# Optimization experiments

Measured on AMD Instinct MI355X. Metric: run time of the kernel, lower is better.

Reference implementation:

```python
import jax, jax.numpy as jnp
import numpy as np

N, E, DIN, ED, H, C = 50000, 800000, 128, 16, 4, 128
HC = H * C
SLOPE = 0.2


def gat_conv(x, ei_src, ei_dst, ea, W, a_src, a_dst, We, a_e, b):
    # x: [N, din]; ea: [E, ed] (self-loops already appended by caller)
    n = x.shape[0]
    h = (x @ W).reshape(n, H, C)                       # [N,H,C]
    al_src = (h * a_src).sum(-1)                       # [N,H]
    al_dst = (h * a_dst).sum(-1)                       # [N,H]
    e = (ea @ We).reshape(-1, H, C)                    # [E,H,C]
    al_e = (e * a_e).sum(-1)                           # [E,H]
    alpha = al_src[ei_src] + al_dst[ei_dst] + al_e     # [E,H]
    alpha = jnp.where(alpha > 0, alpha, SLOPE * alpha)  # LeakyReLU(0.2)
    # per-destination-node segment softmax (stable)
    amax = jax.ops.segment_max(alpha, ei_dst, num_segments=n)
    amax = jnp.where(jnp.isfinite(amax), amax, 0.0)
    ex = jnp.exp(alpha - amax[ei_dst])
    den = jax.ops.segment_sum(ex, ei_dst, num_segments=n)
    alpha = ex / (den[ei_dst] + 1e-16)                 # [E,H]
    msg = h[ei_src] * alpha[:, :, None]                # [E,H,C]
    out = jax.ops.segment_sum(msg, ei_dst, num_segments=n)  # [N,H,C]
    return out.reshape(n, HC) + b


def setup_inputs() -> dict:
    key = jax.random.key(0)
    ks = jax.random.split(key, 16)
    s = 0.05
    inp = {
        "x": jax.random.normal(ks[0], (N, DIN), jnp.float32),
        "edge_index": jax.random.randint(ks[1], (2, E), 0, N, jnp.int64),
        "edge_features": jax.random.normal(ks[2], (E, ED), jnp.float32),
        # layer 1 params
        "W1": jax.random.normal(ks[3], (DIN, HC), jnp.float32) * s,
        "att_src1": jax.random.normal(ks[4], (H, C), jnp.float32) * s,
        "att_dst1": jax.random.normal(ks[5], (H, C), jnp.float32) * s,
        "lin_e1": jax.random.normal(ks[6], (ED, HC), jnp.float32) * s,
        "att_e1": jax.random.normal(ks[7], (H, C), jnp.float32) * s,
        "b1": jnp.zeros((HC,), jnp.float32),
        # layer 2 params
        "W2": jax.random.normal(ks[8], (HC, HC), jnp.float32) * s,
        "att_src2": jax.random.normal(ks[9], (H, C), jnp.float32) * s,
        "att_dst2": jax.random.normal(ks[10], (H, C), jnp.float32) * s,
        "lin_e2": jax.random.normal(ks[11], (ED, HC), jnp.float32) * s,
        "att_e2": jax.random.normal(ks[12], (H, C), jnp.float32) * s,
        "b2": jnp.zeros((HC,), jnp.float32),
    }
    return inp


def reference(x, edge_index, edge_features,
              W1, att_src1, att_dst1, lin_e1, att_e1, b1,
              W2, att_src2, att_dst2, lin_e2, att_e2, b2):
    # add self-loops once (PyG default: add_self_loops=True, edge_attr fill='mean')
    loop = jnp.arange(N, dtype=edge_index.dtype)
    ei_src = jnp.concatenate([edge_index[0], loop])
    ei_dst = jnp.concatenate([edge_index[1], loop])
    mean_ea = edge_features.mean(0)
    ea = jnp.concatenate([edge_features, jnp.broadcast_to(mean_ea, (N, ED))], axis=0)

    h = gat_conv(x, ei_src, ei_dst, ea, W1, att_src1, att_dst1, lin_e1, att_e1, b1)
    h = jax.nn.elu(h)
    h = gat_conv(h, ei_src, ei_dst, ea, W2, att_src2, att_dst2, lin_e2, att_e2, b2)
    return jax.nn.elu(h)
```

## Files before the change

kernel.cpp:

```cpp
#include <hip/hip_runtime.h>
#include <math.h>

#define NNODE 50000
#define NEDGE 800000
#define DINv  128
#define EDv   16
#define NHv   4
#define CHv   128
#define HCv   512
#define SLOPEv 0.2f
#define MEANBLK 512
#define CONVN (NNODE * DINv / 4)

typedef __attribute__((ext_vector_type(8))) short bf16x8;
typedef __attribute__((ext_vector_type(4))) float f32x4;
typedef __attribute__((address_space(3))) unsigned lds_u32;
typedef const __attribute__((address_space(1))) unsigned glb_u32;

__device__ __forceinline__ ushort f2b(float f) {
  unsigned u = __float_as_uint(f);
  u += 0x7FFF + ((u >> 16) & 1);
  return (ushort)(u >> 16);
}
__device__ __forceinline__ float blo(unsigned u) { return __uint_as_float(u << 16); }
__device__ __forceinline__ float bhi(unsigned u) { return __uint_as_float(u & 0xffff0000u); }

__global__ void detect_kernel(const int* __restrict__ ei, int* __restrict__ flag) {
  __shared__ int bad;
  if (threadIdx.x == 0) bad = 0;
  __syncthreads();
  for (int i = threadIdx.x; i < 2048; i += 256)
    if (ei[2 * i + 1] != 0) bad = 1;
  __syncthreads();
  if (threadIdx.x == 0) flag[0] = bad ? 0 : 1;
}

__device__ __forceinline__ int load_idx(const int* __restrict__ ei, int e, int row, int wide) {
  if (wide) return ei[2 * ((size_t)row * NEDGE + e)];
  return ei[(size_t)row * NEDGE + e];
}

__global__ void count_kernel(const int* __restrict__ ei, const int* __restrict__ flag,
                             int* __restrict__ deg) {
  int e = blockIdx.x * blockDim.x + threadIdx.x;
  if (e < NEDGE) {
    int w = flag[0];
    atomicAdd(&deg[load_idx(ei, e, 1, w)], 1);
  }
}

__global__ __launch_bounds__(1024) void scan_kernel(const int* __restrict__ deg,
                                                    int* __restrict__ row_ptr) {
  __shared__ int wsum[16];
  int tid = threadIdx.x;
  int wid = tid >> 6, lane = tid & 63;
  int carry = 0;
  for (int base = 0; base < NNODE; base += 4096) {
    int idx = base + tid * 4;
    int4 x = make_int4(0, 0, 0, 0);
    if (idx < NNODE) x = *(const int4*)(deg + idx);
    int t0 = x.x, t1 = t0 + x.y, t2 = t1 + x.z, t3 = t2 + x.w;
    int v = t3;
#pragma unroll
    for (int off = 1; off < 64; off <<= 1) {
      int t = __shfl_up(v, off, 64);
      if (lane >= off) v += t;
    }
    if (lane == 63) wsum[wid] = v;
    __syncthreads();
    if (wid == 0) {
      int s = (lane < 16) ? wsum[lane] : 0;
#pragma unroll
      for (int off = 1; off < 16; off <<= 1) {
        int t = __shfl_up(s, off, 64);
        if (lane >= off) s += t;
      }
      if (lane < 16) wsum[lane] = s;
    }
    __syncthreads();
    int woff = wid ? wsum[wid - 1] : 0;
    int excl = carry + woff + v - t3;
    if (idx < NNODE) {
      int4 o = make_int4(excl, excl + t0, excl + t1, excl + t2);
      *(int4*)(row_ptr + idx) = o;
    }
    carry += wsum[15];
    __syncthreads();
  }
  if (tid == 0) row_ptr[NNODE] = carry;
}

__global__ void scatter_kernel(const int* __restrict__ ei, const int* __restrict__ flag,
                               const int* __restrict__ row_ptr, int* __restrict__ cursor,
                               int* __restrict__ src_sorted, int* __restrict__ eid_sorted) {
  int e = blockIdx.x * blockDim.x + threadIdx.x;
  if (e < NEDGE) {
    int w = flag[0];
    int d = load_idx(ei, e, 1, w);
    int s = load_idx(ei, e, 0, w);
    int p = row_ptr[d] + atomicAdd(&cursor[d], 1);
    src_sorted[p] = s;
    eid_sorted[p] = e;
  }
}

__global__ void prep_kernel(const float* __restrict__ We1, const float* __restrict__ ae1,
                            const float* __restrict__ We2, const float* __restrict__ ae2,
                            float* __restrict__ v1, float* __restrict__ v2) {
  int t = threadIdx.x;
  int layer = t >> 6, u = t & 63;
  int d = u >> 2, h = u & 3;
  const float* We = layer ? We2 : We1;
  const float* ae = layer ? ae2 : ae1;
  float s = 0.f;
  for (int c = 0; c < CHv; c++) s += We[(size_t)d * HCv + h * CHv + c] * ae[h * CHv + c];
  (layer ? v2 : v1)[d * 4 + h] = s;
}

__global__ void mean_part_kernel(const float* __restrict__ ea, float* __restrict__ partials) {
  float acc[EDv];
#pragma unroll
  for (int d = 0; d < EDv; d++) acc[d] = 0.f;
  int stride = gridDim.x * blockDim.x;
  for (int r = blockIdx.x * blockDim.x + threadIdx.x; r < NEDGE; r += stride) {
    const float4* p = (const float4*)(ea + (size_t)r * EDv);
#pragma unroll
    for (int q = 0; q < 4; q++) {
      float4 v = p[q];
      acc[q * 4 + 0] += v.x; acc[q * 4 + 1] += v.y;
      acc[q * 4 + 2] += v.z; acc[q * 4 + 3] += v.w;
    }
  }
  __shared__ float red[4][EDv];
  int wid = threadIdx.x >> 6, lane = threadIdx.x & 63;
#pragma unroll
  for (int d = 0; d < EDv; d++) {
    float v = acc[d];
    for (int off = 32; off; off >>= 1) v += __shfl_down(v, off, 64);
    if (lane == 0) red[wid][d] = v;
  }
  __syncthreads();
  if (threadIdx.x < EDv) {
    float v = red[0][threadIdx.x] + red[1][threadIdx.x] + red[2][threadIdx.x] + red[3][threadIdx.x];
    partials[blockIdx.x * EDv + threadIdx.x] = v;
  }
}

__global__ void fold_kernel(const float* __restrict__ partials,
                            const float* __restrict__ v1, const float* __restrict__ v2,
                            float* __restrict__ loop1, float* __restrict__ loop2) {
  int tid = threadIdx.x;
  int d = tid & 15, r0 = tid >> 4;
  float v = 0.f;
  for (int r = r0; r < MEANBLK; r += 16) v += partials[r * EDv + d];
  __shared__ float buf[256];
  __shared__ float ms[16];
  buf[tid] = v;
  __syncthreads();
  if (r0 < 8) buf[tid] += buf[tid + 128];
  __syncthreads();
  if (r0 < 4) buf[tid] += buf[tid + 64];
  __syncthreads();
  if (r0 < 2) buf[tid] += buf[tid + 32];
  __syncthreads();
  if (r0 == 0) ms[d] = (buf[tid] + buf[tid + 16]) * (1.0f / NEDGE);
  __syncthreads();
  if (tid < 8) {
    const float* vv = (tid >> 2) ? v2 : v1;
    int h = tid & 3;
    float a = 0.f;
    for (int d2 = 0; d2 < EDv; d2++) a += ms[d2] * vv[d2 * 4 + h];
    ((tid >> 2) ? loop2 : loop1)[h] = a;
  }
}

__global__ void convwt_kernel(const float* __restrict__ x, const float* __restrict__ W1,
                              const float* __restrict__ W2, ushort* __restrict__ xb,
                              ushort* __restrict__ Bt1, ushort* __restrict__ Bt2) {
  int i = blockIdx.x * 256 + threadIdx.x;
  if (i < CONVN) {
    float4 v = ((const float4*)x)[i];
    ushort4 o;
    o.x = f2b(v.x); o.y = f2b(v.y); o.z = f2b(v.z); o.w = f2b(v.w);
    ((ushort4*)xb)[i] = o;
  } else if (i < CONVN + DINv * HCv) {
    int idx = i - CONVN;
    int k = idx >> 9, n = idx & (HCv - 1);
    Bt1[(size_t)n * DINv + k] = f2b(W1[idx]);
  } else if (i < CONVN + DINv * HCv + HCv * HCv) {
    int idx = i - CONVN - DINv * HCv;
    int k = idx >> 9, n = idx & (HCv - 1);
    Bt2[(size_t)n * HCv + k] = f2b(W2[idx]);
  }
}

__global__ void apre1_kernel(const int* __restrict__ src_sorted, const int* __restrict__ eid_sorted,
                             const float* __restrict__ ea, const float* __restrict__ al_src,
                             const float* __restrict__ v1, const float* __restrict__ v2,
                             float* __restrict__ ap1, float* __restrict__ ale2s) {
  __shared__ float sv1[64], sv2[64];
  if (threadIdx.x < 64) sv1[threadIdx.x] = v1[threadIdx.x];
  else if (threadIdx.x < 128) sv2[threadIdx.x - 64] = v2[threadIdx.x - 64];
  __syncthreads();
  int p = blockIdx.x * 256 + threadIdx.x;
  if (p >= NEDGE) return;
  int s = src_sorted[p];
  int e = eid_sorted[p];
  const float4* pr = (const float4*)(ea + (size_t)e * EDv);
  float row[16];
  *(float4*)&row[0] = pr[0]; *(float4*)&row[4] = pr[1];
  *(float4*)&row[8] = pr[2]; *(float4*)&row[12] = pr[3];
  float a0 = 0, a1 = 0, a2 = 0, a3 = 0;
  float b0 = 0, b1 = 0, b2 = 0, b3 = 0;
#pragma unroll
  for (int d = 0; d < 16; d++) {
    a0 += row[d] * sv1[d * 4 + 0];
    a1 += row[d] * sv1[d * 4 + 1];
    a2 += row[d] * sv1[d * 4 + 2];
    a3 += row[d] * sv1[d * 4 + 3];
    b0 += row[d] * sv2[d * 4 + 0];
    b1 += row[d] * sv2[d * 4 + 1];
    b2 += row[d] * sv2[d * 4 + 2];
    b3 += row[d] * sv2[d * 4 + 3];
  }
  float4 as = ((const float4*)al_src)[s];
  ((float4*)ap1)[p] = make_float4(as.x + a0, as.y + a1, as.z + a2, as.w + a3);
  ((float4*)ale2s)[p] = make_float4(b0, b1, b2, b3);
}

__global__ void apre2_kernel(const int* __restrict__ src_sorted, const float* __restrict__ ale2s,
                             const float* __restrict__ al_src, float* __restrict__ ap2) {
  int p = blockIdx.x * 256 + threadIdx.x;
  if (p >= NEDGE) return;
  int s = src_sorted[p];
  float4 a = ((const float4*)al_src)[s];
  float4 b = ((const float4*)ale2s)[p];
  ((float4*)ap2)[p] = make_float4(a.x + b.x, a.y + b.y, a.z + b.z, a.w + b.w);
}

__global__ __launch_bounds__(256) void gemm_mfma_kernel(const ushort* __restrict__ A,
                                                        const ushort* __restrict__ Bt,
                                                        ushort* __restrict__ C, int M, int K,
                                                        const float* __restrict__ a_src,
                                                        const float* __restrict__ a_dst,
                                                        float* __restrict__ al_src,
                                                        float* __restrict__ al_dst) {
  __shared__ ushort As[8][128][8];
  __shared__ ushort Bs[8][128][8];
  __shared__ float ssa[128], ssd[128];
  __shared__ float rsum[2][128][2];
  int tid = threadIdx.x;
  int wid = tid >> 6, lane = tid & 63;

  int nblk = gridDim.x * gridDim.y;
  int j = blockIdx.y * gridDim.x + blockIdx.x;
  int q = nblk >> 3, rem = nblk & 7;
  int xcd = j & 7, idx = j >> 3;
  int d = (xcd < rem) ? xcd * (q + 1) + idx : rem * (q + 1) + (xcd - rem) * q + idx;
  int rb = (d >> 2) * 128, cb = (d & 3) * 128;
  int hblk = cb >> 7;

  int wm = (wid >> 1) * 64, wn = (wid & 1) * 64;
  int lr = lane & 15, lq = lane >> 4;

  if (tid < 128) { ssa[tid] = a_src[cb + tid]; ssd[tid] = a_dst[cb + tid]; }

  f32x4 acc[4][4];
#pragma unroll
  for (int i = 0; i < 4; i++)
#pragma unroll
    for (int jx = 0; jx < 4; jx++) acc[i][jx] = (f32x4){0.f, 0.f, 0.f, 0.f};

  ushort* AsF = &As[0][0][0];
  ushort* BsF = &Bs[0][0][0];

  for (int k0 = 0; k0 < K; k0 += 64) {
#pragma unroll
    for (int s = 0; s < 4; s++) {
      int c = s * 256 + tid;
      int kq = c >> 7, m = c & 127;
      int row = rb + m; if (row >= M) row = M - 1;
      const ushort* gA = A + (size_t)row * K + k0 + kq * 8;
      __builtin_amdgcn_global_load_lds((glb_u32*)gA, (lds_u32*)(AsF + (size_t)c * 8), 16, 0, 0);
    }
#pragma unroll
    for (int s = 0; s < 4; s++) {
      int c = s * 256 + tid;
      int kq = c >> 7, n = c & 127;
      const ushort* gB = Bt + (size_t)(cb + n) * K + k0 + kq * 8;
      __builtin_amdgcn_global_load_lds((glb_u32*)gB, (lds_u32*)(BsF + (size_t)c * 8), 16, 0, 0);
    }
    __syncthreads();
#pragma unroll
    for (int hh = 0; hh < 2; hh++) {
      bf16x8 af[4], bfr[4];
#pragma unroll
      for (int i = 0; i < 4; i++) {
        af[i]  = *(const bf16x8*)&As[hh * 4 + lq][wm + i * 16 + lr][0];
        bfr[i] = *(const bf16x8*)&Bs[hh * 4 + lq][wn + i * 16 + lr][0];
      }
#pragma unroll
      for (int i = 0; i < 4; i++)
#pragma unroll
        for (int jx = 0; jx < 4; jx++)
          acc[i][jx] = __builtin_amdgcn_mfma_f32_16x16x32_bf16(af[i], bfr[jx], acc[i][jx], 0, 0, 0);
    }
    __syncthreads();
  }

#pragma unroll
  for (int i = 0; i < 4; i++) {
    int rbase = rb + wm + i * 16 + lq * 4;
#pragma unroll
    for (int jx = 0; jx < 4; jx++) {
      int col = cb + wn + jx * 16 + lr;
#pragma unroll
      for (int r = 0; r < 4; r++) {
        int row = rbase + r;
        if (row < M) C[(size_t)row * HCv + col] = f2b(acc[i][jx][r]);
      }
    }
  }

  float sa[4], sd[4];
#pragma unroll
  for (int jx = 0; jx < 4; jx++) {
    int c = wn + jx * 16 + lr;
    sa[jx] = ssa[c]; sd[jx] = ssd[c];
  }
#pragma unroll
  for (int i = 0; i < 4; i++) {
#pragma unroll
    for (int r = 0; r < 4; r++) {
      float s1 = 0.f, s2 = 0.f;
#pragma unroll
      for (int jx = 0; jx < 4; jx++) {
        s1 = fmaf(acc[i][jx][r], sa[jx], s1);
        s2 = fmaf(acc[i][jx][r], sd[jx], s2);
      }
#pragma unroll
      for (int off = 1; off < 16; off <<= 1) {
        s1 += __shfl_xor(s1, off, 16);
        s2 += __shfl_xor(s2, off, 16);
      }
      if (lr == 0) {
        int row = wm + i * 16 + lq * 4 + r;
        rsum[0][row][wn >> 6] = s1;
        rsum[1][row][wn >> 6] = s2;
      }
    }
  }
  __syncthreads();
  if (tid < 128) {
    int row = rb + tid;
    if (row < M) {
      al_src[(size_t)row * 4 + hblk] = rsum[0][tid][0] + rsum[0][tid][1];
      al_dst[(size_t)row * 4 + hblk] = rsum[1][tid][0] + rsum[1][tid][1];
    }
  }
}

__device__ __forceinline__ void fma8(float* acc, float w, uint4 u) {
  acc[0] = fmaf(w, blo(u.x), acc[0]);
  acc[1] = fmaf(w, bhi(u.x), acc[1]);
  acc[2] = fmaf(w, blo(u.y), acc[2]);
  acc[3] = fmaf(w, bhi(u.y), acc[3]);
  acc[4] = fmaf(w, blo(u.z), acc[4]);
  acc[5] = fmaf(w, bhi(u.z), acc[5]);
  acc[6] = fmaf(w, blo(u.w), acc[6]);
  acc[7] = fmaf(w, bhi(u.w), acc[7]);
}

__global__ __launch_bounds__(256) void node_kernel(
    const ushort* __restrict__ hb, const float* __restrict__ al_src,
    const float* __restrict__ al_dst, const float* __restrict__ ap,
    const float* __restrict__ loop_al_e, const int* __restrict__ row_ptr,
    const int* __restrict__ src_sorted, const float* __restrict__ bias,
    float* __restrict__ outf, ushort* __restrict__ outb) {
  int wid = threadIdx.x >> 6, lane = threadIdx.x & 63;
  int n = blockIdx.x * 4 + wid;
  if (n >= NNODE) return;
  int base = row_ptr[n];
  int deg = row_ptr[n + 1] - base;
  int h = lane >> 4;
  int jj = lane & 15;

  float aldh = al_dst[(size_t)n * 4 + h];
  float a0 = al_src[(size_t)n * 4 + h] + aldh + loop_al_e[h];
  float alph = a0 > 0.f ? a0 : SLOPEv * a0;
  float wl = __expf(alph);

  uint4 uself = *((const uint4*)(hb + ((size_t)n << 9)) + lane);

  float acc[8];
#pragma unroll
  for (int q = 0; q < 8; q++) acc[q] = 0.f;
  float den = 0.f;

  for (int cs = 0; cs < deg; cs += 16) {
    int cl = min(16, deg - cs);
    float w = 0.f;
    int sv = 0;
    if (jj < cl) {
      int p = base + cs + jj;
      sv = src_sorted[p];
      float a = ap[(size_t)p * 4 + h] + aldh;
      a = a > 0.f ? a : SLOPEv * a;
      w = __expf(a);
      den += w;
    }
    int cl4 = (cl + 3) & ~3;
    for (int j0 = 0; j0 < cl4; j0 += 4) {
      int s0 = __shfl(sv, j0 + 0, 16);
      int s1 = __shfl(sv, j0 + 1, 16);
      int s2 = __shfl(sv, j0 + 2, 16);
      int s3 = __shfl(sv, j0 + 3, 16);
      float w0 = __shfl(w, j0 + 0, 16);
      float w1 = __shfl(w, j0 + 1, 16);
      float w2 = __shfl(w, j0 + 2, 16);
      float w3 = __shfl(w, j0 + 3, 16);
      uint4 u0 = *((const uint4*)(hb + ((size_t)s0 << 9)) + lane);
      uint4 u1 = *((const uint4*)(hb + ((size_t)s1 << 9)) + lane);
      uint4 u2 = *((const uint4*)(hb + ((size_t)s2 << 9)) + lane);
      uint4 u3 = *((const uint4*)(hb + ((size_t)s3 << 9)) + lane);
      fma8(acc, w0, u0);
      fma8(acc, w1, u1);
      fma8(acc, w2, u2);
      fma8(acc, w3, u3);
    }
  }

  fma8(acc, wl, uself);

#pragma unroll
  for (int off = 8; off; off >>= 1) den += __shfl_xor(den, off, 16);
  den += wl;
  float rden = 1.f / (den + 1e-16f);

  const float4* bp = (const float4*)(bias + lane * 8);
  float4 b0 = bp[0], b1 = bp[1];
  float bv[8] = {b0.x, b0.y, b0.z, b0.w, b1.x, b1.y, b1.z, b1.w};
  float r[8];
#pragma unroll
  for (int q = 0; q < 8; q++) {
    float t = acc[q] * rden + bv[q];
    r[q] = t > 0.f ? t : expm1f(t);
  }
  if (outf) {
    float4* op = (float4*)(outf + (size_t)n * HCv + lane * 8);
    op[0] = make_float4(r[0], r[1], r[2], r[3]);
    op[1] = make_float4(r[4], r[5], r[6], r[7]);
  }
  if (outb) {
    uint4 o;
    o.x = (unsigned)f2b(r[0]) | ((unsigned)f2b(r[1]) << 16);
    o.y = (unsigned)f2b(r[2]) | ((unsigned)f2b(r[3]) << 16);
    o.z = (unsigned)f2b(r[4]) | ((unsigned)f2b(r[5]) << 16);
    o.w = (unsigned)f2b(r[6]) | ((unsigned)f2b(r[7]) << 16);
    ((uint4*)(outb + (size_t)n * HCv))[lane] = o;
  }
}

static inline char* take(char*& p, size_t bytes) {
  char* r = p;
  p += (bytes + 255) & ~(size_t)255;
  return r;
}

extern "C" void kernel_launch(void* const* d_in, const int* in_sizes, int n_in,
                              void* d_out, int out_size, void* d_ws, size_t ws_size,
                              hipStream_t stream) {
  (void)in_sizes; (void)n_in; (void)out_size; (void)ws_size;
  const float* x   = (const float*)d_in[0];
  const int*   ei  = (const int*)d_in[1];
  const float* ea  = (const float*)d_in[2];
  const float* W1  = (const float*)d_in[3];
  const float* as1 = (const float*)d_in[4];
  const float* ad1 = (const float*)d_in[5];
  const float* We1 = (const float*)d_in[6];
  const float* ae1 = (const float*)d_in[7];
  const float* b1  = (const float*)d_in[8];
  const float* W2  = (const float*)d_in[9];
  const float* as2 = (const float*)d_in[10];
  const float* ad2 = (const float*)d_in[11];
  const float* We2 = (const float*)d_in[12];
  const float* ae2 = (const float*)d_in[13];
  const float* b2  = (const float*)d_in[14];
  float* out = (float*)d_out;

  char* p = (char*)d_ws;
  ushort* hb        = (ushort*)take(p, (size_t)NNODE * HCv * 2);
  float* al_src     = (float*)take(p, (size_t)NNODE * 4 * 4);
  float* al_dst     = (float*)take(p, (size_t)NNODE * 4 * 4);
  float* ap         = (float*)take(p, (size_t)NEDGE * 4 * 4);
  float* ale2s      = (float*)take(p, (size_t)NEDGE * 4 * 4);
  int*   src_sorted = (int*)take(p, (size_t)NEDGE * 4);
  int*   eid_sorted = (int*)take(p, (size_t)NEDGE * 4);
  int*   row_ptr    = (int*)take(p, (size_t)(NNODE + 1) * 4);
  float* partials   = (float*)take(p, (size_t)MEANBLK * EDv * 4);
  ushort* Bt1       = (ushort*)take(p, (size_t)HCv * DINv * 2);
  ushort* Bt2       = (ushort*)take(p, (size_t)HCv * HCv * 2);
  char* zero_begin = p;
  int*   deg        = (int*)take(p, (size_t)NNODE * 4);
  int*   cursor     = (int*)take(p, (size_t)NNODE * 4);
  size_t zero_len = (size_t)(p - zero_begin);
  float* v1         = (float*)take(p, 64 * 4);
  float* v2         = (float*)take(p, 64 * 4);
  float* loop1      = (float*)take(p, 4 * 4);
  float* loop2      = (float*)take(p, 4 * 4);
  int*   flag       = (int*)take(p, 4);

  ushort* xb  = (ushort*)d_out;
  ushort* h1b = (ushort*)((char*)d_out + (size_t)16 * 1024 * 1024);

  hipMemsetAsync(zero_begin, 0, zero_len, stream);

  detect_kernel<<<1, 256, 0, stream>>>(ei, flag);
  count_kernel<<<(NEDGE + 255) / 256, 256, 0, stream>>>(ei, flag, deg);
  scan_kernel<<<1, 1024, 0, stream>>>(deg, row_ptr);
  scatter_kernel<<<(NEDGE + 255) / 256, 256, 0, stream>>>(ei, flag, row_ptr, cursor,
                                                          src_sorted, eid_sorted);
  prep_kernel<<<1, 128, 0, stream>>>(We1, ae1, We2, ae2, v1, v2);
  mean_part_kernel<<<MEANBLK, 256, 0, stream>>>(ea, partials);
  fold_kernel<<<1, 256, 0, stream>>>(partials, v1, v2, loop1, loop2);
  convwt_kernel<<<(CONVN + DINv * HCv + HCv * HCv + 255) / 256, 256, 0, stream>>>(
      x, W1, W2, xb, Bt1, Bt2);

  gemm_mfma_kernel<<<dim3(HCv / 128, (NNODE + 127) / 128), 256, 0, stream>>>(
      xb, Bt1, hb, NNODE, DINv, as1, ad1, al_src, al_dst);
  apre1_kernel<<<(NEDGE + 255) / 256, 256, 0, stream>>>(src_sorted, eid_sorted, ea, al_src,
                                                        v1, v2, ap, ale2s);
  node_kernel<<<(NNODE + 3) / 4, 256, 0, stream>>>(hb, al_src, al_dst, ap, loop1, row_ptr,
                                                   src_sorted, b1, (float*)nullptr, h1b);

  gemm_mfma_kernel<<<dim3(HCv / 128, (NNODE + 127) / 128), 256, 0, stream>>>(
      h1b, Bt2, hb, NNODE, HCv, as2, ad2, al_src, al_dst);
  apre2_kernel<<<(NEDGE + 255) / 256, 256, 0, stream>>>(src_sorted, ale2s, al_src, ap);
  node_kernel<<<(NNODE + 3) / 4, 256, 0, stream>>>(hb, al_src, al_dst, ap, loop2, row_ptr,
                                                   src_sorted, b2, out, (ushort*)nullptr);
}
```

Before: 720.8 us.

## Merge setup kernels, move src gather into apre1, use nontemporal output stores

Folds the prep, mean-partial and weight/input conversion kernels into one launch, and the scan and fold kernels into one two-block launch, cutting the number of small serial launches. The scatter kernel no longer gathers or writes source indices; apre1 now reads the source index from edge_index through eid_sorted and writes src_sorted itself. Node-kernel outputs use nontemporal 16-byte stores to avoid polluting cache. The trade-off is a dependent gather of ei in apre1 and heterogeneous blocks sharing one launch.

Measured after the change: 709.9 us. No clear change (-1.5%).

```diff
diff --git a/kernel.cpp b/kernel.cpp
--- a/kernel.cpp
+++ b/kernel.cpp
@@ -14,6 +14,7 @@
 
 typedef __attribute__((ext_vector_type(8))) short bf16x8;
 typedef __attribute__((ext_vector_type(4))) float f32x4;
+typedef __attribute__((ext_vector_type(4))) unsigned u32x4;
 typedef __attribute__((address_space(3))) unsigned lds_u32;
 typedef const __attribute__((address_space(1))) unsigned glb_u32;
 
@@ -24,6 +25,12 @@
 }
 __device__ __forceinline__ float blo(unsigned u) { return __uint_as_float(u << 16); }
 __device__ __forceinline__ float bhi(unsigned u) { return __uint_as_float(u & 0xffff0000u); }
+
+__device__ __forceinline__ void nt_store16(void* p, unsigned a, unsigned b, unsigned c,
+                                           unsigned d) {
+  u32x4 t = {a, b, c, d};
+  __builtin_nontemporal_store(t, (u32x4*)p);
+}
 
 __global__ void detect_kernel(const int* __restrict__ ei, int* __restrict__ flag) {
   __shared__ int bad;
@@ -49,163 +56,166 @@
   }
 }
 
-__global__ __launch_bounds__(1024) void scan_kernel(const int* __restrict__ deg,
-                                                    int* __restrict__ row_ptr) {
-  __shared__ int wsum[16];
-  int tid = threadIdx.x;
-  int wid = tid >> 6, lane = tid & 63;
-  int carry = 0;
-  for (int base = 0; base < NNODE; base += 4096) {
-    int idx = base + tid * 4;
-    int4 x = make_int4(0, 0, 0, 0);
-    if (idx < NNODE) x = *(const int4*)(deg + idx);
-    int t0 = x.x, t1 = t0 + x.y, t2 = t1 + x.z, t3 = t2 + x.w;
-    int v = t3;
-#pragma unroll
-    for (int off = 1; off < 64; off <<= 1) {
-      int t = __shfl_up(v, off, 64);
-      if (lane >= off) v += t;
-    }
-    if (lane == 63) wsum[wid] = v;
-    __syncthreads();
-    if (wid == 0) {
-      int s = (lane < 16) ? wsum[lane] : 0;
-#pragma unroll
-      for (int off = 1; off < 16; off <<= 1) {
-        int t = __shfl_up(s, off, 64);
-        if (lane >= off) s += t;
-      }
-      if (lane < 16) wsum[lane] = s;
-    }
-    __syncthreads();
-    int woff = wid ? wsum[wid - 1] : 0;
-    int excl = carry + woff + v - t3;
-    if (idx < NNODE) {
-      int4 o = make_int4(excl, excl + t0, excl + t1, excl + t2);
-      *(int4*)(row_ptr + idx) = o;
-    }
-    carry += wsum[15];
-    __syncthreads();
-  }
-  if (tid == 0) row_ptr[NNODE] = carry;
-}
-
 __global__ void scatter_kernel(const int* __restrict__ ei, const int* __restrict__ flag,
                                const int* __restrict__ row_ptr, int* __restrict__ cursor,
-                               int* __restrict__ src_sorted, int* __restrict__ eid_sorted) {
+                               int* __restrict__ eid_sorted) {
   int e = blockIdx.x * blockDim.x + threadIdx.x;
   if (e < NEDGE) {
     int w = flag[0];
     int d = load_idx(ei, e, 1, w);
-    int s = load_idx(ei, e, 0, w);
     int p = row_ptr[d] + atomicAdd(&cursor[d], 1);
-    src_sorted[p] = s;
     eid_sorted[p] = e;
   }
 }
 
-__global__ void prep_kernel(const float* __restrict__ We1, const float* __restrict__ ae1,
-                            const float* __restrict__ We2, const float* __restrict__ ae2,
-                            float* __restrict__ v1, float* __restrict__ v2) {
-  int t = threadIdx.x;
-  int layer = t >> 6, u = t & 63;
-  int d = u >> 2, h = u & 3;
-  const float* We = layer ? We2 : We1;
-  const float* ae = layer ? ae2 : ae1;
-  float s = 0.f;
-  for (int c = 0; c < CHv; c++) s += We[(size_t)d * HCv + h * CHv + c] * ae[h * CHv + c];
-  (layer ? v2 : v1)[d * 4 + h] = s;
-}
-
-__global__ void mean_part_kernel(const float* __restrict__ ea, float* __restrict__ partials) {
-  float acc[EDv];
-#pragma unroll
-  for (int d = 0; d < EDv; d++) acc[d] = 0.f;
-  int stride = gridDim.x * blockDim.x;
-  for (int r = blockIdx.x * blockDim.x + threadIdx.x; r < NEDGE; r += stride) {
-    const float4* p = (const float4*)(ea + (size_t)r * EDv);
-#pragma unroll
-    for (int q = 0; q < 4; q++) {
-      float4 v = p[q];
-      acc[q * 4 + 0] += v.x; acc[q * 4 + 1] += v.y;
-      acc[q * 4 + 2] += v.z; acc[q * 4 + 3] += v.w;
-    }
-  }
-  __shared__ float red[4][EDv];
-  int wid = threadIdx.x >> 6, lane = threadIdx.x & 63;
-#pragma unroll
-  for (int d = 0; d < EDv; d++) {
-    float v = acc[d];
-    for (int off = 32; off; off >>= 1) v += __shfl_down(v, off, 64);
-    if (lane == 0) red[wid][d] = v;
-  }
-  __syncthreads();
-  if (threadIdx.x < EDv) {
-    float v = red[0][threadIdx.x] + red[1][threadIdx.x] + red[2][threadIdx.x] + red[3][threadIdx.x];
-    partials[blockIdx.x * EDv + threadIdx.x] = v;
-  }
-}
-
-__global__ void fold_kernel(const float* __restrict__ partials,
-                            const float* __restrict__ v1, const float* __restrict__ v2,
-                            float* __restrict__ loop1, float* __restrict__ loop2) {
+__global__ void prep_misc_kernel(const float* __restrict__ ea, float* __restrict__ partials,
+                                 const float* __restrict__ We1, const float* __restrict__ ae1,
+                                 const float* __restrict__ We2, const float* __restrict__ ae2,
+                                 float* __restrict__ v1, float* __restrict__ v2,
+                                 const float* __restrict__ x, const float* __restrict__ W1,
+                                 const float* __restrict__ W2, ushort* __restrict__ xb,
+                                 ushort* __restrict__ Bt1, ushort* __restrict__ Bt2) {
+  int b = blockIdx.x;
+  if (b < MEANBLK) {
+    float acc[EDv];
+#pragma unroll
+    for (int d = 0; d < EDv; d++) acc[d] = 0.f;
+    const int stride = MEANBLK * 256;
+    for (int r = b * 256 + threadIdx.x; r < NEDGE; r += stride) {
+      const float4* p = (const float4*)(ea + (size_t)r * EDv);
+#pragma unroll
+      for (int q = 0; q < 4; q++) {
+        float4 v = p[q];
+        acc[q * 4 + 0] += v.x; acc[q * 4 + 1] += v.y;
+        acc[q * 4 + 2] += v.z; acc[q * 4 + 3] += v.w;
+      }
+    }
+    __shared__ float red[4][EDv];
+    int wid = threadIdx.x >> 6, lane = threadIdx.x & 63;
+#pragma unroll
+    for (int d = 0; d < EDv; d++) {
+      float v = acc[d];
+      for (int off = 32; off; off >>= 1) v += __shfl_down(v, off, 64);
+      if (lane == 0) red[wid][d] = v;
+    }
+    __syncthreads();
+    if (threadIdx.x < EDv) {
+      float v = red[0][threadIdx.x] + red[1][threadIdx.x] + red[2][threadIdx.x] +
+                red[3][threadIdx.x];
+      partials[b * EDv + threadIdx.x] = v;
+    }
+  } else if (b == MEANBLK) {
+    int t = threadIdx.x;
+    if (t < 128) {
+      int layer = t >> 6, u = t & 63;
+      int d = u >> 2, h = u & 3;
+      const float* We = layer ? We2 : We1;
+      const float* ae = layer ? ae2 : ae1;
+      float s = 0.f;
+      for (int c = 0; c < CHv; c++) s += We[(size_t)d * HCv + h * CHv + c] * ae[h * CHv + c];
+      (layer ? v2 : v1)[d * 4 + h] = s;
+    }
+  } else {
+    int i = (b - MEANBLK - 1) * 256 + threadIdx.x;
+    if (i < CONVN) {
+      float4 v = ((const float4*)x)[i];
+      ushort4 o;
+      o.x = f2b(v.x); o.y = f2b(v.y); o.z = f2b(v.z); o.w = f2b(v.w);
+      ((ushort4*)xb)[i] = o;
+    } else if (i < CONVN + DINv * HCv) {
+      int idx = i - CONVN;
+      int k = idx >> 9, n = idx & (HCv - 1);
+      Bt1[(size_t)n * DINv + k] = f2b(W1[idx]);
+    } else if (i < CONVN + DINv * HCv + HCv * HCv) {
+      int idx = i - CONVN - DINv * HCv;
+      int k = idx >> 9, n = idx & (HCv - 1);
+      Bt2[(size_t)n * HCv + k] = f2b(W2[idx]);
+    }
+  }
+}
+
+__global__ __launch_bounds__(1024) void scan_fold_kernel(
+    const int* __restrict__ deg, int* __restrict__ row_ptr,
+    const float* __restrict__ partials, const float* __restrict__ v1,
+    const float* __restrict__ v2, float* __restrict__ loop1, float* __restrict__ loop2) {
   int tid = threadIdx.x;
-  int d = tid & 15, r0 = tid >> 4;
-  float v = 0.f;
-  for (int r = r0; r < MEANBLK; r += 16) v += partials[r * EDv + d];
-  __shared__ float buf[256];
-  __shared__ float ms[16];
-  buf[tid] = v;
-  __syncthreads();
-  if (r0 < 8) buf[tid] += buf[tid + 128];
-  __syncthreads();
-  if (r0 < 4) buf[tid] += buf[tid + 64];
-  __syncthreads();
-  if (r0 < 2) buf[tid] += buf[tid + 32];
-  __syncthreads();
-  if (r0 == 0) ms[d] = (buf[tid] + buf[tid + 16]) * (1.0f / NEDGE);
-  __syncthreads();
-  if (tid < 8) {
-    const float* vv = (tid >> 2) ? v2 : v1;
-    int h = tid & 3;
-    float a = 0.f;
-    for (int d2 = 0; d2 < EDv; d2++) a += ms[d2] * vv[d2 * 4 + h];
-    ((tid >> 2) ? loop2 : loop1)[h] = a;
-  }
-}
-
-__global__ void convwt_kernel(const float* __restrict__ x, const float* __restrict__ W1,
-                              const float* __restrict__ W2, ushort* __restrict__ xb,
-                              ushort* __restrict__ Bt1, ushort* __restrict__ Bt2) {
-  int i = blockIdx.x * 256 + threadIdx.x;
-  if (i < CONVN) {
-    float4 v = ((const float4*)x)[i];
-    ushort4 o;
-    o.x = f2b(v.x); o.y = f2b(v.y); o.z = f2b(v.z); o.w = f2b(v.w);
-    ((ushort4*)xb)[i] = o;
-  } else if (i < CONVN + DINv * HCv) {
-    int idx = i - CONVN;
-    int k = idx >> 9, n = idx & (HCv - 1);
-    Bt1[(size_t)n * DINv + k] = f2b(W1[idx]);
-  } else if (i < CONVN + DINv * HCv + HCv * HCv) {
-    int idx = i - CONVN - DINv * HCv;
-    int k = idx >> 9, n = idx & (HCv - 1);
-    Bt2[(size_t)n * HCv + k] = f2b(W2[idx]);
-  }
-}
-
-__global__ void apre1_kernel(const int* __restrict__ src_sorted, const int* __restrict__ eid_sorted,
+  if (blockIdx.x == 0) {
+    __shared__ int wsum[16];
+    int wid = tid >> 6, lane = tid & 63;
+    int carry = 0;
+    for (int base = 0; base < NNODE; base += 4096) {
+      int idx = base + tid * 4;
+      int4 x = make_int4(0, 0, 0, 0);
+      if (idx < NNODE) x = *(const int4*)(deg + idx);
+      int t0 = x.x, t1 = t0 + x.y, t2 = t1 + x.z, t3 = t2 + x.w;
+      int v = t3;
+#pragma unroll
+      for (int off = 1; off < 64; off <<= 1) {
+        int t = __shfl_up(v, off, 64);
+        if (lane >= off) v += t;
+      }
+      if (lane == 63) wsum[wid] = v;
+      __syncthreads();
+      if (wid == 0) {
+        int s = (lane < 16) ? wsum[lane] : 0;
+#pragma unroll
+        for (int off = 1; off < 16; off <<= 1) {
+          int t = __shfl_up(s, off, 64);
+          if (lane >= off) s += t;
+        }
+        if (lane < 16) wsum[lane] = s;
+      }
+      __syncthreads();
+      int woff = wid ? wsum[wid - 1] : 0;
+      int excl = carry + woff + v - t3;
+      if (idx < NNODE) {
+        int4 o = make_int4(excl, excl + t0, excl + t1, excl + t2);
+        *(int4*)(row_ptr + idx) = o;
+      }
+      carry += wsum[15];
+      __syncthreads();
+    }
+    if (tid == 0) row_ptr[NNODE] = carry;
+  } else {
+    __shared__ float buf[1024];
+    __shared__ float ms[16];
+    int d = tid & 15, r0 = tid >> 4;
+    float v = 0.f;
+    for (int r = r0; r < MEANBLK; r += 64) v += partials[r * EDv + d];
+    buf[tid] = v;
+    __syncthreads();
+#pragma unroll
+    for (int off = 32; off >= 1; off >>= 1) {
+      if (r0 < off) buf[tid] += buf[tid + off * 16];
+      __syncthreads();
+    }
+    if (tid < 16) ms[tid] = buf[tid] * (1.0f / NEDGE);
+    __syncthreads();
+    if (tid < 8) {
+      const float* vv = (tid >> 2) ? v2 : v1;
+      int h = tid & 3;
+      float a = 0.f;
+      for (int d2 = 0; d2 < EDv; d2++) a += ms[d2] * vv[d2 * 4 + h];
+      ((tid >> 2) ? loop2 : loop1)[h] = a;
+    }
+  }
+}
+
+__global__ void apre1_kernel(const int* __restrict__ eid_sorted, const int* __restrict__ ei,
+                             const int* __restrict__ flag,
                              const float* __restrict__ ea, const float* __restrict__ al_src,
                              const float* __restrict__ v1, const float* __restrict__ v2,
-                             float* __restrict__ ap1, float* __restrict__ ale2s) {
+                             float* __restrict__ ap1, float* __restrict__ ale2s,
+                             int* __restrict__ src_sorted) {
   __shared__ float sv1[64], sv2[64];
   if (threadIdx.x < 64) sv1[threadIdx.x] = v1[threadIdx.x];
   else if (threadIdx.x < 128) sv2[threadIdx.x - 64] = v2[threadIdx.x - 64];
   __syncthreads();
   int p = blockIdx.x * 256 + threadIdx.x;
   if (p >= NEDGE) return;
-  int s = src_sorted[p];
   int e = eid_sorted[p];
+  int w = flag[0];
+  int s = load_idx(ei, e, 0, w);
   const float4* pr = (const float4*)(ea + (size_t)e * EDv);
   float row[16];
   *(float4*)&row[0] = pr[0]; *(float4*)&row[4] = pr[1];
@@ -226,6 +236,7 @@
   float4 as = ((const float4*)al_src)[s];
   ((float4*)ap1)[p] = make_float4(as.x + a0, as.y + a1, as.z + a2, as.w + a3);
   ((float4*)ale2s)[p] = make_float4(b0, b1, b2, b3);
+  src_sorted[p] = s;
 }
 
 __global__ void apre2_kernel(const int* __restrict__ src_sorted, const float* __restrict__ ale2s,
@@ -447,17 +458,18 @@
     r[q] = t > 0.f ? t : expm1f(t);
   }
   if (outf) {
-    float4* op = (float4*)(outf + (size_t)n * HCv + lane * 8);
-    op[0] = make_float4(r[0], r[1], r[2], r[3]);
-    op[1] = make_float4(r[4], r[5], r[6], r[7]);
+    float* op = outf + (size_t)n * HCv + lane * 8;
+    nt_store16(op, __float_as_uint(r[0]), __float_as_uint(r[1]),
+               __float_as_uint(r[2]), __float_as_uint(r[3]));
+    nt_store16(op + 4, __float_as_uint(r[4]), __float_as_uint(r[5]),
+               __float_as_uint(r[6]), __float_as_uint(r[7]));
   }
   if (outb) {
-    uint4 o;
-    o.x = (unsigned)f2b(r[0]) | ((unsigned)f2b(r[1]) << 16);
-    o.y = (unsigned)f2b(r[2]) | ((unsigned)f2b(r[3]) << 16);
-    o.z = (unsigned)f2b(r[4]) | ((unsigned)f2b(r[5]) << 16);
-    o.w = (unsigned)f2b(r[6]) | ((unsigned)f2b(r[7]) << 16);
-    ((uint4*)(outb + (size_t)n * HCv))[lane] = o;
+    nt_store16(outb + (size_t)n * HCv + lane * 8,
+               (unsigned)f2b(r[0]) | ((unsigned)f2b(r[1]) << 16),
+               (unsigned)f2b(r[2]) | ((unsigned)f2b(r[3]) << 16),
+               (unsigned)f2b(r[4]) | ((unsigned)f2b(r[5]) << 16),
+               (unsigned)f2b(r[6]) | ((unsigned)f2b(r[7]) << 16));
   }
 }
 
@@ -517,19 +529,15 @@
 
   detect_kernel<<<1, 256, 0, stream>>>(ei, flag);
   count_kernel<<<(NEDGE + 255) / 256, 256, 0, stream>>>(ei, flag, deg);
-  scan_kernel<<<1, 1024, 0, stream>>>(deg, row_ptr);
-  scatter_kernel<<<(NEDGE + 255) / 256, 256, 0, stream>>>(ei, flag, row_ptr, cursor,
-                                                          src_sorted, eid_sorted);
-  prep_kernel<<<1, 128, 0, stream>>>(We1, ae1, We2, ae2, v1, v2);
-  mean_part_kernel<<<MEANBLK, 256, 0, stream>>>(ea, partials);
-  fold_kernel<<<1, 256, 0, stream>>>(partials, v1, v2, loop1, loop2);
-  convwt_kernel<<<(CONVN + DINv * HCv + HCv * HCv + 255) / 256, 256, 0, stream>>>(
-      x, W1, W2, xb, Bt1, Bt2);
+  prep_misc_kernel<<<MEANBLK + 1 + (CONVN + DINv * HCv + HCv * HCv + 255) / 256, 256, 0,
+                     stream>>>(ea, partials, We1, ae1, We2, ae2, v1, v2, x, W1, W2, xb, Bt1, Bt2);
+  scan_fold_kernel<<<2, 1024, 0, stream>>>(deg, row_ptr, partials, v1, v2, loop1, loop2);
+  scatter_kernel<<<(NEDGE + 255) / 256, 256, 0, stream>>>(ei, flag, row_ptr, cursor, eid_sorted);
 
   gemm_mfma_kernel<<<dim3(HCv / 128, (NNODE + 127) / 128), 256, 0, stream>>>(
       xb, Bt1, hb, NNODE, DINv, as1, ad1, al_src, al_dst);
-  apre1_kernel<<<(NEDGE + 255) / 256, 256, 0, stream>>>(src_sorted, eid_sorted, ea, al_src,
-                                                        v1, v2, ap, ale2s);
+  apre1_kernel<<<(NEDGE + 255) / 256, 256, 0, stream>>>(eid_sorted, ei, flag, ea, al_src,
+                                                        v1, v2, ap, ale2s, src_sorted);
   node_kernel<<<(NNODE + 3) / 4, 256, 0, stream>>>(hb, al_src, al_dst, ap, loop1, row_ptr,
                                                    src_sorted, b1, (float*)nullptr, h1b);
 
```
